# Performance work log

Hardware: AMD Instinct MI355X
Metric: run time of the kernel (lower is better)

Reference implementation:

```python
import jax, jax.numpy as jnp
import numpy as np
import math

B, T, E = 1, 2048, 2048
H, D = 16, 128
L = 64
RA_WINDOW = 64
RA_ALPHA = 0.5


def setup_inputs() -> dict:
    key = jax.random.key(0)
    ks = jax.random.split(key, 7)
    s_e = 1.0 / math.sqrt(E)
    s_l = 1.0 / math.sqrt(L)
    return {
        "hidden_states": jax.random.normal(ks[0], (B, T, E), jnp.float32),
        "Wq": jax.random.normal(ks[1], (E, E), jnp.float32) * s_e,       # q_proj.weight [out,in]
        "Wk": jax.random.normal(ks[2], (L, E), jnp.float32) * s_e,       # k_down.weight
        "Wv": jax.random.normal(ks[3], (L, E), jnp.float32) * s_e,       # v_down.weight
        "q_to_latent": jax.random.normal(ks[4], (H, D, L), jnp.float32) * (1.0 / math.sqrt(D)),
        "v_up": jax.random.normal(ks[5], (H, L, D), jnp.float32) * s_l,
        "Wo": jax.random.normal(ks[6], (E, E), jnp.float32) * s_e,       # out_proj.weight
    }


def reference(hidden_states, Wq, Wk, Wv, q_to_latent, v_up, Wo):
    B_, T_, E_ = hidden_states.shape
    NEG = jnp.asarray(-1e30, hidden_states.dtype)

    # per-head queries [B,T,H,D]
    Q = (hidden_states @ Wq.T).reshape(B_, T_, H, D)
    # shared latent K/V [B,T,L]
    latent_k = hidden_states @ Wk.T
    latent_v = hidden_states @ Wv.T

    # per-head Q -> latent alignment [B,T,H,L]
    q_latent = jnp.einsum('bthd,hdl->bthl', Q, q_to_latent)

    inv_sqrt_L = 1.0 / math.sqrt(L)
    # main latent-compressed logits [B,H,T,T]
    logits = jnp.einsum('bthl,bsl->bhts', q_latent, latent_k) * inv_sqrt_L

    i = jnp.arange(T_)[:, None]
    j = jnp.arange(T_)[None, :]
    causal = j <= i                       # [T,T]
    logits = jnp.where(causal[None, None], logits, NEG)

    # reciprocal band pass. NOTE: einsum labels (d vs l) intentionally mismatch,
    # faithfully reproducing the source's outer-product-of-sums computation.
    logits_recip = jnp.einsum('bthd,bsl->bhts', q_latent, latent_k) * inv_sqrt_L
    band = (jnp.abs(i - j) <= RA_WINDOW) & causal
    logits = jnp.where(band[None, None], logits + RA_ALPHA * logits_recip, logits)

    attn = jax.nn.softmax(logits, axis=-1)  # [B,H,T,T]

    # per-head V up-projection [B,T,H,D]
    V_exp = jnp.einsum('btl,hld->bthd', latent_v, v_up)
    ctx = jnp.einsum('bhts,bshd->bthd', attn, V_exp)
    out = ctx.reshape(B_, T_, H * D) @ Wo.T
    return out
```

## Files before the change

### kernel.cpp

```cpp
#include <hip/hip_runtime.h>


#define T_ 2048
#define E_ 2048
#define H_ 16
#define D_ 128
#define L_ 64
#define NQ 1152

typedef float  floatx4 __attribute__((ext_vector_type(4)));
typedef __bf16 bf16x8  __attribute__((ext_vector_type(8)));

__device__ __forceinline__ ushort f2b(float x){
  unsigned int u = __float_as_uint(x);
  u = (u + 0x7fffu + ((u >> 16) & 1u)) >> 16;
  return (ushort)u;
}
__device__ __forceinline__ float blo(unsigned int u){ return __uint_as_float(u << 16); }
__device__ __forceinline__ float bhi(unsigned int u){ return __uint_as_float(u & 0xffff0000u); }

__device__ __forceinline__ void glds16(const ushort* g, ushort* l){
#if __has_builtin(__builtin_amdgcn_global_load_lds)
  __builtin_amdgcn_global_load_lds((const __attribute__((address_space(1))) void*)g,
                                   (__attribute__((address_space(3))) void*)l, 16, 0, 0);
#else
  *(uint4*)l = *(const uint4*)g;
#endif
}

__global__ __launch_bounds__(256)
void k_f2b4(const float* __restrict__ a, ushort* __restrict__ oa,
            const float* __restrict__ b, ushort* __restrict__ ob,
            const float* __restrict__ c, ushort* __restrict__ oc,
            const float* __restrict__ d, ushort* __restrict__ od){
  int bid = blockIdx.x; const float* src; ushort* dst; int base;
  if (bid < 4096){ src=a; dst=oa; base=bid; }
  else if (bid < 8192){ src=b; dst=ob; base=bid-4096; }
  else if (bid < 8320){ src=c; dst=oc; base=bid-8192; }
  else { src=d; dst=od; base=bid-8320; }
  int i = (base*256 + (int)threadIdx.x)*4;
  float4 v = *(const float4*)(src + i);
  ushort4 o; o.x=f2b(v.x); o.y=f2b(v.y); o.z=f2b(v.z); o.w=f2b(v.w);
  *(ushort4*)(dst + i) = o;
}

__global__ __launch_bounds__(128)
void k_prep_wql(const float* __restrict__ Wq, const float* __restrict__ q2l,
                ushort* __restrict__ Wql){
  const int h = blockIdx.z, lh = blockIdx.y;
  const int e = blockIdx.x*128 + threadIdx.x;
  const float* qb = q2l + (size_t)h*D_*L_ + lh*32;
  float acc[32];
  #pragma unroll
  for (int i=0;i<32;++i) acc[i]=0.f;
  for (int d=0; d<128; ++d){
    float wv = Wq[(size_t)(h*128+d)*E_ + e];
    #pragma unroll
    for (int i=0;i<32;++i) acc[i] += wv*qb[(size_t)d*64 + i];
  }
  #pragma unroll
  for (int i=0;i<32;++i) Wql[(size_t)(h*64 + lh*32 + i)*E_ + e] = f2b(acc[i]);
}

__global__ __launch_bounds__(256)
void k_prep_vupT(const float* __restrict__ vup, ushort* __restrict__ vupT){
  const int h = blockIdx.x, tid = threadIdx.x;
  for (int idx = tid; idx < L_*D_; idx += 256){
    int l = idx >> 7, d = idx & 127;
    vupT[(size_t)h*D_*L_ + d*64 + l] = f2b(vup[(size_t)h*L_*D_ + idx]);
  }
}

template<int MT,int NT,bool OB16>
__global__ __launch_bounds__(256)
void gemm_glds(const ushort* __restrict__ A, const ushort* __restrict__ B,
               float* __restrict__ Cf, ushort* __restrict__ Cb,
               int M, int N, int K, float scale){
  constexpr int BM = 32*MT, BN = 32*NT;
  constexpr int IA = BM/64, IB = BN/64;
  __shared__ ushort As[BM*32];
  __shared__ ushort Bs[BN*32];
  const int tid = threadIdx.x, lane = tid&63, wv = tid>>6;
  const int wm = wv & 1, wn = wv >> 1;
  const int l15 = lane&15, quad = lane>>4;
  const int m0 = blockIdx.y*BM, n0 = blockIdx.x*BN;
  const float sc = (n0 < 1024) ? scale : 1.0f;
  floatx4 acc[MT][NT] = {};
  for (int k0=0; k0<K; k0+=32){
    __syncthreads();
    #pragma unroll
    for (int j=0;j<IA;++j){
      int c = (j*4 + wv)*64 + lane; int row = c>>2, kc = (c&3)*8;
      glds16(A + (size_t)(m0+row)*K + k0 + kc, &As[c*8]);
    }
    #pragma unroll
    for (int j=0;j<IB;++j){
      int c = (j*4 + wv)*64 + lane; int row = c>>2, kc = (c&3)*8;
      glds16(B + (size_t)(n0+row)*K + k0 + kc, &Bs[c*8]);
    }
    __syncthreads();
    bf16x8 af[MT], bfr[NT];
    #pragma unroll
    for (int mi=0;mi<MT;++mi)
      af[mi] = *(const bf16x8*)(&As[(wm*MT*16 + mi*16 + l15)*32 + quad*8]);
    #pragma unroll
    for (int ni=0;ni<NT;++ni)
      bfr[ni] = *(const bf16x8*)(&Bs[(wn*NT*16 + ni*16 + l15)*32 + quad*8]);
    #pragma unroll
    for (int mi=0;mi<MT;++mi)
      #pragma unroll
      for (int ni=0;ni<NT;++ni)
        acc[mi][ni] = __builtin_amdgcn_mfma_f32_16x16x32_bf16(af[mi], bfr[ni], acc[mi][ni], 0,0,0);
  }
  #pragma unroll
  for (int mi=0;mi<MT;++mi){
    const int rb = m0 + wm*MT*16 + mi*16 + quad*4;
    #pragma unroll
    for (int ni=0;ni<NT;++ni){
      const int col = n0 + wn*NT*16 + ni*16 + l15;
      #pragma unroll
      for (int r=0;r<4;++r){
        if constexpr (OB16) Cb[(size_t)(rb+r)*N + col] = f2b(acc[mi][ni][r]*sc);
        else                Cf[(size_t)(rb+r)*N + col] = acc[mi][ni][r];
      }
    }
  }
}

__global__ __launch_bounds__(256)
void k_rowsums(const ushort* __restrict__ qkvb,
               float* __restrict__ rsq, float* __restrict__ rsk){
  int i = blockIdx.x*256 + threadIdx.x;
  const ushort* src; float* dst;
  if (i < T_*H_){
    int t = i>>4, g = i&15;
    src = qkvb + (size_t)t*NQ + g*64; dst = rsq + i;
  } else {
    int t = i - T_*H_;
    if (t >= T_) return;
    src = qkvb + (size_t)t*NQ + 1024; dst = rsk + t;
  }
  const uint4* p = (const uint4*)src;
  float s = 0.f;
  #pragma unroll
  for (int j=0;j<8;++j){
    uint4 u = p[j];
    const unsigned int uu[4] = {u.x,u.y,u.z,u.w};
    #pragma unroll
    for (int q=0;q<4;++q){ s += blo(uu[q]); s += bhi(uu[q]); }
  }
  *dst = s;
}

__global__ __launch_bounds__(256)
void k_vexp_mfma(const ushort* __restrict__ qkvb, const ushort* __restrict__ vupT,
                 ushort* __restrict__ vexpT){
  const int h = blockIdx.y, t0 = blockIdx.x*64;
  const int tid = threadIdx.x, lane = tid&63, w = tid>>6;
  const int l15 = lane&15, quad = lane>>4;
  bf16x8 a[2][2], b[4][2];
  #pragma unroll
  for (int mt=0;mt<2;++mt)
    #pragma unroll
    for (int kk=0;kk<2;++kk)
      a[mt][kk] = *(const bf16x8*)(vupT + (size_t)h*D_*L_ + (w*32+mt*16+l15)*64 + kk*32 + quad*8);
  #pragma unroll
  for (int nt=0;nt<4;++nt)
    #pragma unroll
    for (int kk=0;kk<2;++kk)
      b[nt][kk] = *(const bf16x8*)(qkvb + (size_t)(t0+nt*16+l15)*NQ + 1088 + kk*32 + quad*8);
  floatx4 acc[2][4] = {};
  #pragma unroll
  for (int mt=0;mt<2;++mt)
    #pragma unroll
    for (int nt=0;nt<4;++nt)
      #pragma unroll
      for (int kk=0;kk<2;++kk)
        acc[mt][nt] = __builtin_amdgcn_mfma_f32_16x16x32_bf16(a[mt][kk], b[nt][kk], acc[mt][nt], 0,0,0);
  #pragma unroll
  for (int mt=0;mt<2;++mt)
    #pragma unroll
    for (int nt=0;nt<4;++nt)
      #pragma unroll
      for (int r=0;r<4;++r)
        vexpT[((size_t)h*D_ + w*32+mt*16+quad*4+r)*T_ + t0 + nt*16 + l15] = f2b(acc[mt][nt][r]);
}

__global__ __launch_bounds__(256, 4)
void k_attn(const ushort* __restrict__ qkvb,
            const float*  __restrict__ rsq,
            const float*  __restrict__ rsk,
            const ushort* __restrict__ vexpT,
            ushort*       __restrict__ ctx,
            ushort*       __restrict__ partO,
            float*        __restrict__ partML,
            int CH){
  constexpr int PP = 72;
  __shared__ ushort Ks[64*64];
  __shared__ ushort Vts[128*64];
  __shared__ ushort Ps[4][16*PP];
  const int h  = blockIdx.y;
  const int bxr = (int)gridDim.x - 1 - (int)blockIdx.x;
  int qt, c;
  if (CH == 8){
    if (bxr < 8){ qt = bxr; c = 0; }
    else if (bxr < 24){ int u = bxr-8;  qt = 8  + (u>>1); c = u&1; }
    else if (bxr < 48){ int u = bxr-24; qt = 16 + u/3;    c = u - (u/3)*3; }
    else               { int u = bxr-48; qt = 24 + (u>>2); c = u&3; }
  } else { qt = bxr; c = 0; }
  const int nct = (qt + CH) / CH;
  const int stBeg = c*CH, stEnd = min(qt, stBeg + CH - 1);
  const int t0 = qt*64;
  const int tid = threadIdx.x, lane = tid & 63, w = tid >> 6;
  const int l15 = lane & 15, quad = lane >> 4;

  const int qrow = t0 + w*16 + l15;
  const bf16x8 q0 = *(const bf16x8*)(qkvb + (size_t)qrow*NQ + h*64 + quad*8);
  const bf16x8 q1 = *(const bf16x8*)(qkvb + (size_t)qrow*NQ + h*64 + 32 + quad*8);
  const float rqv = rsq[(size_t)qrow*H_ + h] * 0.5f;

  float mrun = -INFINITY, lrun = 0.f;
  floatx4 o[8] = {};

  for (int st=stBeg; st<=stEnd; ++st){
    const int s0 = st*64;
    __syncthreads();
    #pragma unroll
    for (int j=0;j<2;++j){ int cc = tid + j*256;
      int row = cc>>3, kc = ((cc&7) ^ (row&7))*8;
      glds16(qkvb + (size_t)(s0 + row)*NQ + 1024 + kc, &Ks[cc*8]); }
    #pragma unroll
    for (int j=0;j<4;++j){ int cc = tid + j*256;
      int row = cc>>3, sc2 = ((cc&7) ^ (row&7))*8;
      glds16(vexpT + ((size_t)h*128 + row)*T_ + s0 + sc2, &Vts[cc*8]); }
    __syncthreads();
    floatx4 sT[4] = {};
    #pragma unroll
    for (int jt=0;jt<4;++jt){
      const int srow = jt*16 + l15, sx = srow & 7;
      bf16x8 k0f = *(const bf16x8*)(&Ks[srow*64 + (quad^sx)*8]);
      sT[jt] = __builtin_amdgcn_mfma_f32_16x16x32_bf16(k0f, q0, sT[jt], 0,0,0);
      bf16x8 k1f = *(const bf16x8*)(&Ks[srow*64 + ((4+quad)^sx)*8]);
      sT[jt] = __builtin_amdgcn_mfma_f32_16x16x32_bf16(k1f, q1, sT[jt], 0,0,0);
    }
    float mloc = -3.0e38f;
    if (st >= qt-1){
      #pragma unroll
      for (int jt=0;jt<4;++jt){
        const float4 rk4 = *(const float4*)(rsk + s0 + jt*16 + quad*4);
        #pragma unroll
        for (int r=0;r<4;++r){
          const int sg = s0 + jt*16 + quad*4 + r;
          const int dd = qrow - sg;
          float x = sT[jt][r];
          x = (dd <= 64) ? x + rqv*((const float*)&rk4)[r] : x;
          x = (dd < 0)   ? -3.0e38f : x;
          sT[jt][r] = x; mloc = fmaxf(mloc, x);
        }
      }
    } else {
      #pragma unroll
      for (int jt=0;jt<4;++jt)
        #pragma unroll
        for (int r=0;r<4;++r) mloc = fmaxf(mloc, sT[jt][r]);
    }
    mloc = fmaxf(mloc, __shfl_xor(mloc, 16));
    mloc = fmaxf(mloc, __shfl_xor(mloc, 32));
    const float mn = fmaxf(mrun, mloc);
    const float al = exp2f(mrun - mn);
    float ss = 0.f;
    #pragma unroll
    for (int jt=0;jt<4;++jt)
      #pragma unroll
      for (int r=0;r<4;++r){
        float p = exp2f(sT[jt][r]-mn); sT[jt][r] = p; ss += p;
      }
    ss += __shfl_xor(ss, 16); ss += __shfl_xor(ss, 32);
    lrun = lrun*al + ss; mrun = mn;
    #pragma unroll
    for (int jt=0;jt<4;++jt){
      ushort4 pw; pw.x=f2b(sT[jt][0]); pw.y=f2b(sT[jt][1]);
      pw.z=f2b(sT[jt][2]); pw.w=f2b(sT[jt][3]);
      *(ushort4*)(&Ps[w][l15*PP + jt*16 + quad*4]) = pw;
    }
    if (__any(al < 1.0f)){
      float alr[4];
      #pragma unroll
      for (int r=0;r<4;++r) alr[r] = __shfl(al, quad*4 + r);
      #pragma unroll
      for (int nt=0;nt<8;++nt){
        o[nt][0]*=alr[0]; o[nt][1]*=alr[1]; o[nt][2]*=alr[2]; o[nt][3]*=alr[3];
      }
    }
    #pragma unroll
    for (int kks=0;kks<2;++kks){
      bf16x8 pf = *(const bf16x8*)(&Ps[w][l15*PP + kks*32 + quad*8]);
      #pragma unroll
      for (int nt=0;nt<8;++nt){
        const int vrow = nt*16 + l15, vx = vrow & 7;
        bf16x8 vf = *(const bf16x8*)(&Vts[vrow*64 + ((kks*4+quad)^vx)*8]);
        o[nt] = __builtin_amdgcn_mfma_f32_16x16x32_bf16(pf, vf, o[nt], 0,0,0);
      }
    }
  }
  const float linv = 1.f/lrun;
  float lr4[4];
  #pragma unroll
  for (int r=0;r<4;++r) lr4[r] = __shfl(linv, quad*4 + r);
  if (nct == 1){
    #pragma unroll
    for (int r=0;r<4;++r){
      const int row = t0 + w*16 + quad*4 + r;
      #pragma unroll
      for (int nt=0;nt<8;++nt)
        ctx[(size_t)row*E_ + h*D_ + nt*16 + l15] = f2b(o[nt][r]*lr4[r]);
    }
  } else {
    const int slot = (h*24 + (qt-8))*4 + c;
    ushort* po = partO + (size_t)slot*8192;
    #pragma unroll
    for (int nt=0;nt<8;++nt)
      #pragma unroll
      for (int r=0;r<4;++r)
        po[((w*8+nt)*4+r)*64 + quad*16 + l15] = f2b(o[nt][r]*lr4[r]);
    if (quad == 0){
      float2 ml; ml.x = mrun; ml.y = lrun;
      ((float2*)partML)[(size_t)slot*64 + w*16 + l15] = ml;
    }
  }
}

__global__ __launch_bounds__(256)
void k_merge(const ushort* __restrict__ partO, const float* __restrict__ partML,
             ushort* __restrict__ ctx){
  const int h = blockIdx.y, qt = 8 + blockIdx.x;
  const int nct = (qt + 8) / 8;
  const int tid = threadIdx.x;
  const int rg = tid >> 2, d0 = (tid & 3)*32;
  const int w = rg >> 4, quad = (rg >> 2) & 3, rr = rg & 3;
  const int n0 = d0 >> 4;
  const int sbase = (h*24 + (qt-8))*4;
  float m[4], l[4], M = -INFINITY;
  for (int c=0;c<4;++c){
    if (c < nct){
      float2 v = ((const float2*)partML)[(size_t)(sbase+c)*64 + rg];
      m[c]=v.x; l[c]=v.y; M = fmaxf(M, v.x);
    }
  }
  float lt = 0.f, wgt[4];
  for (int c=0;c<4;++c){
    if (c < nct){ wgt[c] = exp2f(m[c]-M)*l[c]; lt += wgt[c]; }
  }
  const float inv = 1.f/lt;
  float acc[32];
  #pragma unroll
  for (int i=0;i<32;++i) acc[i]=0.f;
  for (int c=0;c<4;++c){
    if (c >= nct) break;
    const float sc = wgt[c]*inv;
    const ushort* po = partO + (size_t)(sbase+c)*8192;
    #pragma unroll
    for (int nn=0;nn<2;++nn){
      const ushort* p2 = po + ((w*8 + n0+nn)*4 + rr)*64 + quad*16;
      uint4 u  = *(const uint4*)p2;
      uint4 u2 = *(const uint4*)(p2 + 8);
      const unsigned int uu[8] = {u.x,u.y,u.z,u.w,u2.x,u2.y,u2.z,u2.w};
      #pragma unroll
      for (int q=0;q<8;++q){
        acc[nn*16+q*2]   += sc*blo(uu[q]);
        acc[nn*16+q*2+1] += sc*bhi(uu[q]);
      }
    }
  }
  ushort* dst = ctx + (size_t)(qt*64 + rg)*E_ + h*D_ + d0;
  #pragma unroll
  for (int k=0;k<8;++k){
    ushort4 ov; ov.x=f2b(acc[k*4]); ov.y=f2b(acc[k*4+1]);
    ov.z=f2b(acc[k*4+2]); ov.w=f2b(acc[k*4+3]);
    *(ushort4*)(dst + k*4) = ov;
  }
}

extern "C" void kernel_launch(void* const* d_in, const int* in_sizes, int n_in,
                              void* d_out, int out_size, void* d_ws, size_t ws_size,
                              hipStream_t stream) {
  const float* hs  = (const float*)d_in[0];
  const float* Wq  = (const float*)d_in[1];
  const float* Wk  = (const float*)d_in[2];
  const float* Wv  = (const float*)d_in[3];
  const float* q2l = (const float*)d_in[4];
  const float* vup = (const float*)d_in[5];
  const float* Wo  = (const float*)d_in[6];
  float* out = (float*)d_out;
  char* ws = (char*)d_ws;

  ushort* hsb   = (ushort*)(ws + 0);
  ushort* Wqkvb = (ushort*)(ws + 8388608);
  ushort* Wob   = (ushort*)(ws + 13107200);
  ushort* qkvb  = (ushort*)(ws + 21495808);
  ushort* vupT  = (ushort*)(ws + 26214400);
  float*  rsqp  = (float*) (ws + 26476544);
  float*  rskp  = (float*) (ws + 26607616);
  ushort* vexpT = (ushort*)(ws + 26615808);
  ushort* ctxb  = (ushort*)(ws + 35004416);
  ushort* partO = (ushort*)(ws + 43393024);
  float*  partML= (float*) (ws + 68558848);
  const size_t NEED = 69345280;
  const int CH = (ws_size >= NEED) ? 8 : 32;

  k_f2b4<<<8448, 256, 0, stream>>>(hs, hsb, Wo, Wob,
                                   Wk, Wqkvb + (size_t)1024*E_,
                                   Wv, Wqkvb + (size_t)1088*E_);

  k_prep_wql<<<dim3(16,2,16), 128, 0, stream>>>(Wq, q2l, Wqkvb);
  k_prep_vupT<<<16, 256, 0, stream>>>(vup, vupT);

  gemm_glds<2,2,true><<<dim3(18,32), 256, 0, stream>>>(
      hsb, Wqkvb, nullptr, qkvb, T_, NQ, E_, 0.18033688f);

  k_rowsums<<<136, 256, 0, stream>>>(qkvb, rsqp, rskp);

  k_vexp_mfma<<<dim3(32,16), 256, 0, stream>>>(qkvb, vupT, vexpT);

  k_attn<<<dim3(CH==8 ? 80 : 32, 16), 256, 0, stream>>>(
      qkvb, rsqp, rskp, vexpT, ctxb, partO, partML, CH);

  if (CH == 8)
    k_merge<<<dim3(24,16), 256, 0, stream>>>(partO, partML, ctxb);

  gemm_glds<2,4,false><<<dim3(16,32), 256, 0, stream>>>(
      ctxb, Wob, out, nullptr, T_, E_, E_, 1.0f);
}
```

Baseline: 270.4 us.

## Use split-K GEMMs with reduction kernels for QKV and output projections

Replaces the QKV projection and output projection GEMMs with split-K variants using larger 128x128 tiles. Partial fp32 results are summed in separate reduction kernels, and the QKV reduction also computes the row sums, replacing k_rowsums. The workspace is re-laid out so buffers alias each other and the whole plan fits the split path. The goal is more blocks in flight and more reuse per tile, at the cost of extra fp32 partial-sum traffic and additional launches.

```diff
diff --git a/kernel.cpp b/kernel.cpp
--- a/kernel.cpp
+++ b/kernel.cpp
@@ -68,6 +68,60 @@
   for (int idx = tid; idx < L_*D_; idx += 256){
     int l = idx >> 7, d = idx & 127;
     vupT[(size_t)h*D_*L_ + d*64 + l] = f2b(vup[(size_t)h*L_*D_ + idx]);
+  }
+}
+
+template<int MT,int NT>
+__global__ __launch_bounds__(256)
+void gemm_splitk(const ushort* __restrict__ A, const ushort* __restrict__ B,
+                 float* __restrict__ P, int M, int N, int K, int Klen){
+  constexpr int BM = 32*MT, BN = 32*NT;
+  constexpr int IA = BM/64, IB = BN/64;
+  __shared__ ushort As[BM*32];
+  __shared__ ushort Bs[BN*32];
+  const int tid = threadIdx.x, lane = tid&63, wv = tid>>6;
+  const int wm = wv & 1, wn = wv >> 1;
+  const int l15 = lane&15, quad = lane>>4;
+  const int m0 = blockIdx.y*BM, n0 = blockIdx.x*BN;
+  const int kbeg = blockIdx.z*Klen, kend = kbeg + Klen;
+  floatx4 acc[MT][NT] = {};
+  for (int k0=kbeg; k0<kend; k0+=32){
+    __syncthreads();
+    #pragma unroll
+    for (int j=0;j<IA;++j){
+      int c = (j*4 + wv)*64 + lane; int row = c>>2, kc = (c&3)*8;
+      glds16(A + (size_t)(m0+row)*K + k0 + kc, &As[c*8]);
+    }
+    #pragma unroll
+    for (int j=0;j<IB;++j){
+      int c = (j*4 + wv)*64 + lane; int row = c>>2, kc = (c&3)*8;
+      glds16(B + (size_t)(n0+row)*K + k0 + kc, &Bs[c*8]);
+    }
+    __syncthreads();
+    bf16x8 af[MT], bfr[NT];
+    #pragma unroll
+    for (int mi=0;mi<MT;++mi)
+      af[mi] = *(const bf16x8*)(&As[(wm*MT*16 + mi*16 + l15)*32 + quad*8]);
+    #pragma unroll
+    for (int ni=0;ni<NT;++ni)
+      bfr[ni] = *(const bf16x8*)(&Bs[(wn*NT*16 + ni*16 + l15)*32 + quad*8]);
+    #pragma unroll
+    for (int mi=0;mi<MT;++mi)
+      #pragma unroll
+      for (int ni=0;ni<NT;++ni)
+        acc[mi][ni] = __builtin_amdgcn_mfma_f32_16x16x32_bf16(af[mi], bfr[ni], acc[mi][ni], 0,0,0);
+  }
+  float* Pz = P + (size_t)blockIdx.z*M*N;
+  #pragma unroll
+  for (int mi=0;mi<MT;++mi){
+    const int rb = m0 + wm*MT*16 + mi*16 + quad*4;
+    #pragma unroll
+    for (int ni=0;ni<NT;++ni){
+      const int col = n0 + wn*NT*16 + ni*16 + l15;
+      #pragma unroll
+      for (int r=0;r<4;++r)
+        Pz[(size_t)(rb+r)*N + col] = acc[mi][ni][r];
+    }
   }
 }
 
@@ -125,6 +179,47 @@
       }
     }
   }
+}
+
+__global__ __launch_bounds__(256)
+void k_reduce_qkv(const float* __restrict__ P, ushort* __restrict__ qkvb,
+                  float* __restrict__ rsq, float* __restrict__ rsk,
+                  float scale){
+  const int t = blockIdx.x, tid = threadIdx.x;
+  const float4* r0 = (const float4*)(P + (size_t)t*NQ);
+  const size_t ZS = (size_t)T_*NQ/4;
+  float4 a = r0[tid], b = r0[tid+ZS], c = r0[tid+2*ZS], d = r0[tid+3*ZS];
+  float x0 = (a.x+b.x+c.x+d.x)*scale;
+  float x1 = (a.y+b.y+c.y+d.y)*scale;
+  float x2 = (a.z+b.z+c.z+d.z)*scale;
+  float x3 = (a.w+b.w+c.w+d.w)*scale;
+  ushort4 o; o.x=f2b(x0); o.y=f2b(x1); o.z=f2b(x2); o.w=f2b(x3);
+  *(ushort4*)(qkvb + (size_t)t*NQ + tid*4) = o;
+  float s = x0+x1+x2+x3;
+  s += __shfl_xor(s,1); s += __shfl_xor(s,2);
+  s += __shfl_xor(s,4); s += __shfl_xor(s,8);
+  if ((tid & 15) == 0) rsq[(size_t)t*H_ + (tid>>4)] = s;
+  if (tid < 32){
+    const int c2 = 256 + tid;
+    float4 a2 = r0[c2], b2 = r0[c2+ZS], c4 = r0[c2+2*ZS], d2 = r0[c2+3*ZS];
+    float y0 = a2.x+b2.x+c4.x+d2.x, y1 = a2.y+b2.y+c4.y+d2.y;
+    float y2 = a2.z+b2.z+c4.z+d2.z, y3 = a2.w+b2.w+c4.w+d2.w;
+    ushort4 o2; o2.x=f2b(y0); o2.y=f2b(y1); o2.z=f2b(y2); o2.w=f2b(y3);
+    *(ushort4*)(qkvb + (size_t)t*NQ + 1024 + tid*4) = o2;
+    float s2 = y0+y1+y2+y3;
+    s2 += __shfl_xor(s2,1); s2 += __shfl_xor(s2,2);
+    s2 += __shfl_xor(s2,4); s2 += __shfl_xor(s2,8);
+    if (tid == 0) rsk[t] = s2;
+  }
+}
+
+__global__ __launch_bounds__(256)
+void k_reduce_out(const float* __restrict__ P, float* __restrict__ out){
+  const size_t i = ((size_t)blockIdx.x*256 + threadIdx.x)*4;
+  float4 a = *(const float4*)(P + i);
+  float4 b = *(const float4*)(P + i + (size_t)T_*E_);
+  float4 o; o.x=a.x+b.x; o.y=a.y+b.y; o.z=a.z+b.z; o.w=a.w+b.w;
+  *(float4*)(out + i) = o;
 }
 
 __global__ __launch_bounds__(256)
@@ -394,19 +489,21 @@
   float* out = (float*)d_out;
   char* ws = (char*)d_ws;
 
-  ushort* hsb   = (ushort*)(ws + 0);
-  ushort* Wqkvb = (ushort*)(ws + 8388608);
-  ushort* Wob   = (ushort*)(ws + 13107200);
+  ushort* Wob   = (ushort*)(ws + 0);
+  ushort* hsb   = (ushort*)(ws + 8388608);
+  ushort* ctxb  = (ushort*)(ws + 8388608);
+  ushort* Wqkvb = (ushort*)(ws + 16777216);
+  float*  rsqp  = (float*) (ws + 16777216);
+  float*  rskp  = (float*) (ws + 16908288);
   ushort* qkvb  = (ushort*)(ws + 21495808);
   ushort* vupT  = (ushort*)(ws + 26214400);
-  float*  rsqp  = (float*) (ws + 26476544);
-  float*  rskp  = (float*) (ws + 26607616);
-  ushort* vexpT = (ushort*)(ws + 26615808);
-  ushort* ctxb  = (ushort*)(ws + 35004416);
-  ushort* partO = (ushort*)(ws + 43393024);
-  float*  partML= (float*) (ws + 68558848);
-  const size_t NEED = 69345280;
-  const int CH = (ws_size >= NEED) ? 8 : 32;
+  float*  qkvP  = (float*) (ws + 26476544);
+  ushort* vexpT = (ushort*)(ws + 26476544);
+  float*  outP  = (float*) (ws + 26476544);
+  ushort* partO = (ushort*)(ws + 34865152);
+  float*  partML= (float*) (ws + 60030976);
+  const size_t NEED = 64225280;
+  const bool SPLIT = (ws_size >= NEED);
 
   k_f2b4<<<8448, 256, 0, stream>>>(hs, hsb, Wo, Wob,
                                    Wk, Wqkvb + (size_t)1024*E_,
@@ -415,19 +512,31 @@
   k_prep_wql<<<dim3(16,2,16), 128, 0, stream>>>(Wq, q2l, Wqkvb);
   k_prep_vupT<<<16, 256, 0, stream>>>(vup, vupT);
 
-  gemm_glds<2,2,true><<<dim3(18,32), 256, 0, stream>>>(
-      hsb, Wqkvb, nullptr, qkvb, T_, NQ, E_, 0.18033688f);
-
-  k_rowsums<<<136, 256, 0, stream>>>(qkvb, rsqp, rskp);
+  if (SPLIT){
+    gemm_splitk<4,4><<<dim3(9,16,4), 256, 0, stream>>>(
+        hsb, Wqkvb, qkvP, T_, NQ, E_, 512);
+    k_reduce_qkv<<<2048, 256, 0, stream>>>(qkvP, qkvb, rsqp, rskp, 0.18033688f);
+  } else {
+    gemm_glds<2,2,true><<<dim3(18,32), 256, 0, stream>>>(
+        hsb, Wqkvb, nullptr, qkvb, T_, NQ, E_, 0.18033688f);
+    k_rowsums<<<136, 256, 0, stream>>>(qkvb, rsqp, rskp);
+  }
 
   k_vexp_mfma<<<dim3(32,16), 256, 0, stream>>>(qkvb, vupT, vexpT);
 
-  k_attn<<<dim3(CH==8 ? 80 : 32, 16), 256, 0, stream>>>(
+  const int CH = SPLIT ? 8 : 32;
+  k_attn<<<dim3(SPLIT ? 80 : 32, 16), 256, 0, stream>>>(
       qkvb, rsqp, rskp, vexpT, ctxb, partO, partML, CH);
 
-  if (CH == 8)
+  if (SPLIT)
     k_merge<<<dim3(24,16), 256, 0, stream>>>(partO, partML, ctxb);
 
-  gemm_glds<2,4,false><<<dim3(16,32), 256, 0, stream>>>(
-      ctxb, Wob, out, nullptr, T_, E_, E_, 1.0f);
-}
+  if (SPLIT){
+    gemm_splitk<4,4><<<dim3(16,16,2), 256, 0, stream>>>(
+        ctxb, Wob, outP, T_, E_, E_, 1024);
+    k_reduce_out<<<4096, 256, 0, stream>>>(outP, out);
+  } else {
+    gemm_glds<2,4,false><<<dim3(16,32), 256, 0, stream>>>(
+        ctxb, Wob, out, nullptr, T_, E_, E_, 1.0f);
+  }
+}
```

Result: slower. 275.9 us (+2.0%).

## Double-buffer GEMM loads, pipeline attention K/V staging, enlarge GEMM tiles

Applied to the files above, without the earlier changes.

The GEMM kernel now double-buffers its LDS tiles. It prefetches the next K-slice with global_load_lds while the current slice is computed, using explicit vmcnt waits and raw barriers, and it remaps block ids into an interleaved order. Tile sizes are doubled in M (4x2 and 4x4 warp tiles), which halves the grid. The attention kernel overlaps loading the next K tile with softmax, and the next V tile with the end of the PV step, and raises wave priority around the MFMA sections. This targets exposed global-load latency, at the cost of more LDS per block, fewer blocks on the smaller GEMM, and fragile hand-counted vmcnt values.

```diff
diff --git a/kernel.cpp b/kernel.cpp
--- a/kernel.cpp
+++ b/kernel.cpp
@@ -26,6 +26,13 @@
 #else
   *(uint4*)l = *(const uint4*)g;
 #endif
+}
+
+template<int N> __device__ __forceinline__ void vmwait(){
+  if constexpr (N==0) asm volatile("s_waitcnt vmcnt(0)" ::: "memory");
+  if constexpr (N==2) asm volatile("s_waitcnt vmcnt(2)" ::: "memory");
+  if constexpr (N==3) asm volatile("s_waitcnt vmcnt(3)" ::: "memory");
+  if constexpr (N==4) asm volatile("s_waitcnt vmcnt(4)" ::: "memory");
 }
 
 __global__ __launch_bounds__(256)
@@ -73,44 +80,60 @@
 
 template<int MT,int NT,bool OB16>
 __global__ __launch_bounds__(256)
-void gemm_glds(const ushort* __restrict__ A, const ushort* __restrict__ B,
+void gemm_pipe(const ushort* __restrict__ A, const ushort* __restrict__ B,
                float* __restrict__ Cf, ushort* __restrict__ Cb,
                int M, int N, int K, float scale){
   constexpr int BM = 32*MT, BN = 32*NT;
   constexpr int IA = BM/64, IB = BN/64;
-  __shared__ ushort As[BM*32];
-  __shared__ ushort Bs[BN*32];
+  constexpr int NLD = IA+IB;
+  __shared__ ushort As[2][BM*32];
+  __shared__ ushort Bs[2][BN*32];
   const int tid = threadIdx.x, lane = tid&63, wv = tid>>6;
   const int wm = wv & 1, wn = wv >> 1;
   const int l15 = lane&15, quad = lane>>4;
-  const int m0 = blockIdx.y*BM, n0 = blockIdx.x*BN;
+  const int nbx = gridDim.x;
+  const int nwg = nbx * (int)gridDim.y;
+  int bid = (int)blockIdx.y*nbx + (int)blockIdx.x;
+  bid = (bid & 7)*(nwg >> 3) + (bid >> 3);
+  const int m0 = (bid / nbx)*BM, n0 = (bid % nbx)*BN;
   const float sc = (n0 < 1024) ? scale : 1.0f;
-  floatx4 acc[MT][NT] = {};
-  for (int k0=0; k0<K; k0+=32){
-    __syncthreads();
+
+  auto STAGE = [&](int buf, int k0){
     #pragma unroll
     for (int j=0;j<IA;++j){
       int c = (j*4 + wv)*64 + lane; int row = c>>2, kc = (c&3)*8;
-      glds16(A + (size_t)(m0+row)*K + k0 + kc, &As[c*8]);
+      glds16(A + (size_t)(m0+row)*K + k0 + kc, &As[buf][c*8]);
     }
     #pragma unroll
     for (int j=0;j<IB;++j){
       int c = (j*4 + wv)*64 + lane; int row = c>>2, kc = (c&3)*8;
-      glds16(B + (size_t)(n0+row)*K + k0 + kc, &Bs[c*8]);
-    }
-    __syncthreads();
+      glds16(B + (size_t)(n0+row)*K + k0 + kc, &Bs[buf][c*8]);
+    }
+  };
+
+  floatx4 acc[MT][NT] = {};
+  STAGE(0, 0);
+  for (int k0=0; k0<K; k0+=32){
+    const int cur = (k0>>5)&1;
+    const bool more = (k0+32 < K);
+    if (more) STAGE(cur^1, k0+32);
+    if (more) vmwait<NLD>(); else vmwait<0>();
+    __builtin_amdgcn_s_barrier();
+    __builtin_amdgcn_sched_barrier(0);
     bf16x8 af[MT], bfr[NT];
     #pragma unroll
     for (int mi=0;mi<MT;++mi)
-      af[mi] = *(const bf16x8*)(&As[(wm*MT*16 + mi*16 + l15)*32 + quad*8]);
+      af[mi] = *(const bf16x8*)(&As[cur][(wm*MT*16 + mi*16 + l15)*32 + quad*8]);
     #pragma unroll
     for (int ni=0;ni<NT;++ni)
-      bfr[ni] = *(const bf16x8*)(&Bs[(wn*NT*16 + ni*16 + l15)*32 + quad*8]);
+      bfr[ni] = *(const bf16x8*)(&Bs[cur][(wn*NT*16 + ni*16 + l15)*32 + quad*8]);
     #pragma unroll
     for (int mi=0;mi<MT;++mi)
       #pragma unroll
       for (int ni=0;ni<NT;++ni)
         acc[mi][ni] = __builtin_amdgcn_mfma_f32_16x16x32_bf16(af[mi], bfr[ni], acc[mi][ni], 0,0,0);
+    __builtin_amdgcn_sched_barrier(0);
+    if (more) __builtin_amdgcn_s_barrier();
   }
   #pragma unroll
   for (int mi=0;mi<MT;++mi){
@@ -214,6 +237,19 @@
   const int tid = threadIdx.x, lane = tid & 63, w = tid >> 6;
   const int l15 = lane & 15, quad = lane >> 4;
 
+  auto stageK = [&](int s0k){
+    #pragma unroll
+    for (int j=0;j<2;++j){ int cc = tid + j*256;
+      int row = cc>>3, kc = ((cc&7) ^ (row&7))*8;
+      glds16(qkvb + (size_t)(s0k + row)*NQ + 1024 + kc, &Ks[cc*8]); }
+  };
+  auto stageV = [&](int s0v){
+    #pragma unroll
+    for (int j=0;j<4;++j){ int cc = tid + j*256;
+      int row = cc>>3, sc2 = ((cc&7) ^ (row&7))*8;
+      glds16(vexpT + ((size_t)h*128 + row)*T_ + s0v + sc2, &Vts[cc*8]); }
+  };
+
   const int qrow = t0 + w*16 + l15;
   const bf16x8 q0 = *(const bf16x8*)(qkvb + (size_t)qrow*NQ + h*64 + quad*8);
   const bf16x8 q1 = *(const bf16x8*)(qkvb + (size_t)qrow*NQ + h*64 + 32 + quad*8);
@@ -222,19 +258,16 @@
   float mrun = -INFINITY, lrun = 0.f;
   floatx4 o[8] = {};
 
+  stageK(stBeg*64); stageV(stBeg*64);
+
   for (int st=stBeg; st<=stEnd; ++st){
     const int s0 = st*64;
-    __syncthreads();
-    #pragma unroll
-    for (int j=0;j<2;++j){ int cc = tid + j*256;
-      int row = cc>>3, kc = ((cc&7) ^ (row&7))*8;
-      glds16(qkvb + (size_t)(s0 + row)*NQ + 1024 + kc, &Ks[cc*8]); }
-    #pragma unroll
-    for (int j=0;j<4;++j){ int cc = tid + j*256;
-      int row = cc>>3, sc2 = ((cc&7) ^ (row&7))*8;
-      glds16(vexpT + ((size_t)h*128 + row)*T_ + s0 + sc2, &Vts[cc*8]); }
-    __syncthreads();
+    const bool more = (st < stEnd);
+    asm volatile("s_waitcnt vmcnt(4)" ::: "memory");
+    __builtin_amdgcn_s_barrier();
+    __builtin_amdgcn_sched_barrier(0);
     floatx4 sT[4] = {};
+    __builtin_amdgcn_s_setprio(1);
     #pragma unroll
     for (int jt=0;jt<4;++jt){
       const int srow = jt*16 + l15, sx = srow & 7;
@@ -243,6 +276,10 @@
       bf16x8 k1f = *(const bf16x8*)(&Ks[srow*64 + ((4+quad)^sx)*8]);
       sT[jt] = __builtin_amdgcn_mfma_f32_16x16x32_bf16(k1f, q1, sT[jt], 0,0,0);
     }
+    __builtin_amdgcn_s_setprio(0);
+    __builtin_amdgcn_sched_barrier(0);
+    __builtin_amdgcn_s_barrier();
+    if (more) stageK(s0 + 64);
     float mloc = -3.0e38f;
     if (st >= qt-1){
       #pragma unroll
@@ -292,6 +329,12 @@
         o[nt][0]*=alr[0]; o[nt][1]*=alr[1]; o[nt][2]*=alr[2]; o[nt][3]*=alr[3];
       }
     }
+    __builtin_amdgcn_sched_barrier(0);
+    if (more) asm volatile("s_waitcnt vmcnt(2)" ::: "memory");
+    else      asm volatile("s_waitcnt vmcnt(0)" ::: "memory");
+    __builtin_amdgcn_s_barrier();
+    __builtin_amdgcn_sched_barrier(0);
+    __builtin_amdgcn_s_setprio(1);
     #pragma unroll
     for (int kks=0;kks<2;++kks){
       bf16x8 pf = *(const bf16x8*)(&Ps[w][l15*PP + kks*32 + quad*8]);
@@ -301,6 +344,12 @@
         bf16x8 vf = *(const bf16x8*)(&Vts[vrow*64 + ((kks*4+quad)^vx)*8]);
         o[nt] = __builtin_amdgcn_mfma_f32_16x16x32_bf16(pf, vf, o[nt], 0,0,0);
       }
+    }
+    __builtin_amdgcn_s_setprio(0);
+    __builtin_amdgcn_sched_barrier(0);
+    if (more){
+      __builtin_amdgcn_s_barrier();
+      stageV(s0 + 64);
     }
   }
   const float linv = 1.f/lrun;
@@ -415,7 +464,7 @@
   k_prep_wql<<<dim3(16,2,16), 128, 0, stream>>>(Wq, q2l, Wqkvb);
   k_prep_vupT<<<16, 256, 0, stream>>>(vup, vupT);
 
-  gemm_glds<2,2,true><<<dim3(18,32), 256, 0, stream>>>(
+  gemm_pipe<4,2,true><<<dim3(18,16), 256, 0, stream>>>(
       hsb, Wqkvb, nullptr, qkvb, T_, NQ, E_, 0.18033688f);
 
   k_rowsums<<<136, 256, 0, stream>>>(qkvb, rsqp, rskp);
@@ -428,6 +477,6 @@
   if (CH == 8)
     k_merge<<<dim3(24,16), 256, 0, stream>>>(partO, partML, ctxb);
 
-  gemm_glds<2,4,false><<<dim3(16,32), 256, 0, stream>>>(
+  gemm_pipe<4,4,false><<<dim3(16,16), 256, 0, stream>>>(
       ctxb, Wob, out, nullptr, T_, E_, E_, 1.0f);
 }
```

New measurement: 304.4 us. 1.13x slower.

## Software-pipeline K/V LDS staging across attention tiles with split barriers

Applied to the files above, without the earlier changes.

Restructures the attention loop so the next tile's K is loaded into LDS right after the QK MFMAs and the next V right after the PV MFMAs. Explicit vmcnt waits and finer barriers replace the two full __syncthreads per tile. s_setprio is raised around the MFMA blocks. The aim is to hide global-to-LDS latency behind compute. The risk is that the hand-counted vmcnt values are fragile: the loader issues 2 K and 4 V global_load_lds per thread, and any miscount is a data race.

```diff
diff --git a/kernel.cpp b/kernel.cpp
--- a/kernel.cpp
+++ b/kernel.cpp
@@ -214,6 +214,19 @@
   const int tid = threadIdx.x, lane = tid & 63, w = tid >> 6;
   const int l15 = lane & 15, quad = lane >> 4;
 
+  auto stageK = [&](int s0k){
+    #pragma unroll
+    for (int j=0;j<2;++j){ int cc = tid + j*256;
+      int row = cc>>3, kc = ((cc&7) ^ (row&7))*8;
+      glds16(qkvb + (size_t)(s0k + row)*NQ + 1024 + kc, &Ks[cc*8]); }
+  };
+  auto stageV = [&](int s0v){
+    #pragma unroll
+    for (int j=0;j<4;++j){ int cc = tid + j*256;
+      int row = cc>>3, sc2 = ((cc&7) ^ (row&7))*8;
+      glds16(vexpT + ((size_t)h*128 + row)*T_ + s0v + sc2, &Vts[cc*8]); }
+  };
+
   const int qrow = t0 + w*16 + l15;
   const bf16x8 q0 = *(const bf16x8*)(qkvb + (size_t)qrow*NQ + h*64 + quad*8);
   const bf16x8 q1 = *(const bf16x8*)(qkvb + (size_t)qrow*NQ + h*64 + 32 + quad*8);
@@ -222,19 +235,16 @@
   float mrun = -INFINITY, lrun = 0.f;
   floatx4 o[8] = {};
 
+  stageK(stBeg*64); stageV(stBeg*64);
+
   for (int st=stBeg; st<=stEnd; ++st){
     const int s0 = st*64;
-    __syncthreads();
-    #pragma unroll
-    for (int j=0;j<2;++j){ int cc = tid + j*256;
-      int row = cc>>3, kc = ((cc&7) ^ (row&7))*8;
-      glds16(qkvb + (size_t)(s0 + row)*NQ + 1024 + kc, &Ks[cc*8]); }
-    #pragma unroll
-    for (int j=0;j<4;++j){ int cc = tid + j*256;
-      int row = cc>>3, sc2 = ((cc&7) ^ (row&7))*8;
-      glds16(vexpT + ((size_t)h*128 + row)*T_ + s0 + sc2, &Vts[cc*8]); }
-    __syncthreads();
+    const bool more = (st < stEnd);
+    asm volatile("s_waitcnt vmcnt(4)" ::: "memory");
+    __builtin_amdgcn_s_barrier();
+    __builtin_amdgcn_sched_barrier(0);
     floatx4 sT[4] = {};
+    __builtin_amdgcn_s_setprio(1);
     #pragma unroll
     for (int jt=0;jt<4;++jt){
       const int srow = jt*16 + l15, sx = srow & 7;
@@ -243,6 +253,10 @@
       bf16x8 k1f = *(const bf16x8*)(&Ks[srow*64 + ((4+quad)^sx)*8]);
       sT[jt] = __builtin_amdgcn_mfma_f32_16x16x32_bf16(k1f, q1, sT[jt], 0,0,0);
     }
+    __builtin_amdgcn_s_setprio(0);
+    __builtin_amdgcn_sched_barrier(0);
+    __builtin_amdgcn_s_barrier();
+    if (more) stageK(s0 + 64);
     float mloc = -3.0e38f;
     if (st >= qt-1){
       #pragma unroll
@@ -292,6 +306,12 @@
         o[nt][0]*=alr[0]; o[nt][1]*=alr[1]; o[nt][2]*=alr[2]; o[nt][3]*=alr[3];
       }
     }
+    __builtin_amdgcn_sched_barrier(0);
+    if (more) asm volatile("s_waitcnt vmcnt(2)" ::: "memory");
+    else      asm volatile("s_waitcnt vmcnt(0)" ::: "memory");
+    __builtin_amdgcn_s_barrier();
+    __builtin_amdgcn_sched_barrier(0);
+    __builtin_amdgcn_s_setprio(1);
     #pragma unroll
     for (int kks=0;kks<2;++kks){
       bf16x8 pf = *(const bf16x8*)(&Ps[w][l15*PP + kks*32 + quad*8]);
@@ -301,6 +321,12 @@
         bf16x8 vf = *(const bf16x8*)(&Vts[vrow*64 + ((kks*4+quad)^vx)*8]);
         o[nt] = __builtin_amdgcn_mfma_f32_16x16x32_bf16(pf, vf, o[nt], 0,0,0);
       }
+    }
+    __builtin_amdgcn_s_setprio(0);
+    __builtin_amdgcn_sched_barrier(0);
+    if (more){
+      __builtin_amdgcn_s_barrier();
+      stageV(s0 + 64);
     }
   }
   const float linv = 1.f/lrun;
```

Measured after the change: 270.7 us. No clear change (+0.1%).
